# Performance work log

Hardware: AMD Instinct MI355X
Metric: run time of the kernel (lower is better)

The kernel has to match this reference:

```python
import jax, jax.numpy as jnp
import numpy as np

D_MODEL = 1024
NUM_HEADS = 16
HDIM = D_MODEL // NUM_HEADS
THETA = 10000.0


def setup_inputs() -> dict:
    key = jax.random.key(0)
    ks = jax.random.split(key, 5)
    bs, seq = 4, 2048
    std = np.sqrt(2.0 / (D_MODEL + D_MODEL))
    def w(k):
        # trunc_normal approximated by clipped normal (same distribution family)
        return jnp.clip(std * jax.random.normal(k, (D_MODEL, D_MODEL), jnp.float32), -3 * std, 3 * std)
    return {
        "x": jax.random.normal(ks[0], (bs, seq, D_MODEL), jnp.float32),
        "Wq": w(ks[1]), "Wk": w(ks[2]), "Wv": w(ks[3]), "Wo": w(ks[4]),
        "token_positions": jnp.arange(seq, dtype=jnp.int64),
    }


def _rope(x, token_positions):
    # x: (bs, H, S, hdim); rotate even/odd interleaved pairs
    inv_freq = THETA ** (-2.0 * jnp.arange(HDIM // 2, dtype=jnp.float32) / HDIM)
    freqs = token_positions.astype(jnp.float32)[:, None] * inv_freq[None, :]  # (S, hdim/2)
    cos, sin = jnp.cos(freqs), jnp.sin(freqs)
    x_even, x_odd = x[..., 0::2], x[..., 1::2]
    out_even = x_even * cos - x_odd * sin
    out_odd = x_odd * cos + x_even * sin
    # interleave back: stack on new last axis then reshape
    return jnp.stack([out_even, out_odd], axis=-1).reshape(x.shape)


def reference(x, Wq, Wk, Wv, Wo, token_positions):
    bs, seq, _ = x.shape
    q = (x @ Wq.T).reshape(bs, seq, NUM_HEADS, HDIM).transpose(0, 2, 1, 3)
    k = (x @ Wk.T).reshape(bs, seq, NUM_HEADS, HDIM).transpose(0, 2, 1, 3)
    v = (x @ Wv.T).reshape(bs, seq, NUM_HEADS, HDIM).transpose(0, 2, 1, 3)
    q = _rope(q, token_positions)
    k = _rope(k, token_positions)
    scores = jnp.einsum("bhsd,bhtd->bhst", q, k) / jnp.sqrt(jnp.float32(HDIM))
    mask = jnp.tril(jnp.ones((seq, seq), dtype=bool))
    scores = jnp.where(mask, scores, -jnp.inf)
    attn = jax.nn.softmax(scores, axis=-1)
    out = jnp.einsum("bhst,bhtd->bhsd", attn, v)
    out = out.transpose(0, 2, 1, 3).reshape(bs, seq, D_MODEL)
    return out @ Wo.T
```

## Files before the change

### kernel.cpp

```cpp
#include <hip/hip_runtime.h>
#include <hip/hip_fp16.h>

typedef _Float16 half8 __attribute__((ext_vector_type(8)));
typedef _Float16 half4 __attribute__((ext_vector_type(4)));
typedef _Float16 half2v __attribute__((ext_vector_type(2)));
typedef float f32x4 __attribute__((ext_vector_type(4)));
typedef float f32x8v __attribute__((ext_vector_type(8)));
typedef float f32x16 __attribute__((ext_vector_type(16)));

#define SEQ   2048
#define DM    1024
#define NH    16
#define HD    64
#define BSZ   4

#if __has_builtin(__builtin_amdgcn_exp2f)
#define EXP2(x) __builtin_amdgcn_exp2f(x)
#else
#define EXP2(x) exp2f(x)
#endif

#define QSCALE 0.1803368801f
#define ROPE_C 0.41524101186f

__device__ __forceinline__ void gload16(const void* g, void* l) {
  __builtin_amdgcn_global_load_lds((const __attribute__((address_space(1))) void*)g,
                                   (__attribute__((address_space(3))) void*)l,
                                   16, 0, 0);
}

__global__ void cvtAll(const float* __restrict__ x,
                       const float* __restrict__ s0, const float* __restrict__ s1,
                       const float* __restrict__ s2, const float* __restrict__ s3,
                       _Float16* __restrict__ xh, _Float16* __restrict__ dqkv,
                       _Float16* __restrict__ dO) {
  const int i = blockIdx.x * blockDim.x + threadIdx.x;
  const float* src;
  _Float16* dst;
  int idx;
  if (i < 2097152) {
    src = x; dst = xh; idx = i;
  } else {
    const int j = i - 2097152;
    const int which = j >> 18;
    idx = j & 262143;
    src = (which == 0) ? s0 : (which == 1) ? s1 : (which == 2) ? s2 : s3;
    dst = (which < 3) ? (dqkv + (long)which * (1u << 20)) : dO;
  }
  float4 v = ((const float4*)src)[idx];
  half4 o = { (_Float16)v.x, (_Float16)v.y, (_Float16)v.z, (_Float16)v.w };
  ((half4*)dst)[idx] = o;
}

template<int MODE>
__global__ __launch_bounds__(256)
void gemm_hk(const _Float16* __restrict__ A, const _Float16* __restrict__ B,
             _Float16* __restrict__ oQ, _Float16* __restrict__ oK,
             _Float16* __restrict__ oVt, float* __restrict__ oF,
             const int* __restrict__ tp) {
  __shared__ _Float16 As[2][128*32];
  __shared__ _Float16 Bs[2][128*32];
  const int tid  = threadIdx.x;
  const int wid  = tid >> 6, lane = tid & 63;
  const int wm   = wid >> 1, wn = wid & 1;
  const int fr   = lane & 15, fg = lane >> 4;
  const long m0  = (long)blockIdx.x * 128;
  const long n0  = (long)blockIdx.y * 128;
  const int sg    = (lane & 7) ^ ((lane >> 3) & 7);
  const int srowl = 2*(lane >> 3) + (sg >> 2);
  const int scol  = (sg & 3) * 8;
  const _Float16* ga0 = A + (m0 + wid*32 + srowl) * 1024 + scol;
  const _Float16* gb0 = B + (n0 + wid*32 + srowl) * 1024 + scol;
  const int lofs = wid*32*32;

  f32x4 acc[4][4] = {};

  auto ldfrag = [&](const char* base, int R) -> half8 {
    const int r = R & 31, r2 = r >> 1;
    return *(const half8*)(base + (R >> 5)*2048 + r2*128 +
                           (((((r & 1) << 2) | fg) ^ (r2 & 7)) << 4));
  };

  gload16(ga0,           &As[0][lofs]);
  gload16(ga0 + 16*1024, &As[0][lofs + 16*32]);
  gload16(gb0,           &Bs[0][lofs]);
  gload16(gb0 + 16*1024, &Bs[0][lofs + 16*32]);
  __syncthreads();

  int cur = 0;
  for (int k0 = 0; k0 < 1024; k0 += 32) {
    if (k0 + 32 < 1024) {
      gload16(ga0 + k0 + 32,           &As[cur^1][lofs]);
      gload16(ga0 + k0 + 32 + 16*1024, &As[cur^1][lofs + 16*32]);
      gload16(gb0 + k0 + 32,           &Bs[cur^1][lofs]);
      gload16(gb0 + k0 + 32 + 16*1024, &Bs[cur^1][lofs + 16*32]);
    }
    const char* Ab = (const char*)&As[cur][0];
    const char* Bb = (const char*)&Bs[cur][0];
    half8 af[4], bf[4];
#pragma unroll
    for (int i = 0; i < 4; ++i) {
      af[i] = ldfrag(Ab, wm*64 + i*16 + fr);
      bf[i] = ldfrag(Bb, wn*64 + i*16 + fr);
    }
    __builtin_amdgcn_s_setprio(1);
#pragma unroll
    for (int i = 0; i < 4; ++i)
#pragma unroll
      for (int j = 0; j < 4; ++j)
        acc[i][j] = __builtin_amdgcn_mfma_f32_16x16x32_f16(af[i], bf[j], acc[i][j], 0, 0, 0);
    __builtin_amdgcn_s_setprio(0);
    __syncthreads();
    cur ^= 1;
  }

  if (MODE == 0) {
    const int which = (int)(n0 >> 10);
    const int nloc0 = ((int)n0 & 1023) + wn*64;
    const bool odd = fr & 1;
#pragma unroll
    for (int i = 0; i < 4; ++i) {
      const long r0 = m0 + wm*64 + i*16 + fg*4;
      const int  bb = (int)(r0 >> 11);
      const int  s  = (int)(r0 & 2047);
#pragma unroll
      for (int j = 0; j < 4; ++j) {
        const int nl = nloc0 + j*16 + fr;
        const int h  = nl >> 6, d = nl & 63;
        const long bh = (long)(bb*NH + h);
        if (which == 2) {
          half4 pk = { (_Float16)acc[i][j][0], (_Float16)acc[i][j][1],
                       (_Float16)acc[i][j][2], (_Float16)acc[i][j][3] };
          *(half4*)&oVt[(bh*HD + d)*SEQ + s] = pk;
        } else {
          const float inv = exp2f(-ROPE_C * (float)(d >> 1));
#pragma unroll
          for (int r = 0; r < 4; ++r) {
            const float v = acc[i][j][r];
            const float p = __shfl_xor(v, 1);
            float sn, cs;
            __sincosf((float)tp[s + r] * inv, &sn, &cs);
            const float out = odd ? (v*cs + p*sn) : (v*cs - p*sn);
            if (which == 0)
              oQ[(bh*SEQ + s + r)*HD + d] = (_Float16)(out * QSCALE);
            else
              oK[(bh*SEQ + s + r)*HD + d] = (_Float16)out;
          }
        }
      }
    }
  } else {
#pragma unroll
    for (int i = 0; i < 4; ++i) {
      const long r0 = m0 + wm*64 + i*16 + fg*4;
#pragma unroll
      for (int j = 0; j < 4; ++j) {
        const long col = n0 + wn*64 + j*16 + fr;
#pragma unroll
        for (int r = 0; r < 4; ++r)
          oF[(r0 + r)*DM + col] = acc[i][j][r];
      }
    }
  }
}

__global__ __launch_bounds__(256, 2)
void fattn(const _Float16* __restrict__ Q, const _Float16* __restrict__ K,
           const _Float16* __restrict__ Vt, _Float16* __restrict__ O) {
  __shared__ _Float16 Ks[2][64*64];
  __shared__ _Float16 Vs[2][64*64];
  const int tid = threadIdx.x, wid = tid >> 6, lane = tid & 63;
  const int q31 = lane & 31, hi = lane >> 5;
  const int qp  = (q31 & 19) | ((q31 & 4) << 1) | ((q31 & 8) >> 1);
  const int bh = blockIdx.x, b = bh >> 4, h = bh & 15;
  const int y = blockIdx.y;
  const int qs_[2] = { (15 - y)*128 + wid*32, y*128 + wid*32 };
  const _Float16* Qb = Q + (long)bh * SEQ * HD;
  const _Float16* Kb = K + (long)bh * SEQ * HD;
  const _Float16* Vb = Vt + (long)bh * HD * SEQ;

  half8 qf[2][4];
#pragma unroll
  for (int s = 0; s < 2; ++s)
#pragma unroll
    for (int c = 0; c < 4; ++c)
      qf[s][c] = *(const half8*)&Qb[(qs_[s] + q31)*HD + c*16 + hi*8];

  f32x16 oacc[2][2] = {};
  float m_s[2] = { -1e30f, -1e30f }, l_s[2] = { 0.f, 0.f };

  const int srow = lane >> 3;
  const int sc16 = (lane & 7) ^ srow;
  const int r1 = wid*16 + srow, r2 = r1 + 8;

  const int nt = (15 - y)*2 + 2;

  gload16(Kb + (long)r1*HD + sc16*8, &Ks[0][(wid*16)*64]);
  gload16(Kb + (long)r2*HD + sc16*8, &Ks[0][(wid*16 + 8)*64]);
  gload16(Vb + (long)r1*SEQ + sc16*8, &Vs[0][(wid*16)*64]);
  gload16(Vb + (long)r2*SEQ + sc16*8, &Vs[0][(wid*16 + 8)*64]);
  __syncthreads();

  int cur = 0;
  for (int t = 0; t < nt; ++t) {
    const int kv0 = t * 64;

    if (t + 1 < nt) {
      const int nkv = kv0 + 64;
      gload16(Kb + (long)(nkv + r1)*HD + sc16*8, &Ks[cur^1][(wid*16)*64]);
      gload16(Kb + (long)(nkv + r2)*HD + sc16*8, &Ks[cur^1][(wid*16 + 8)*64]);
      gload16(Vb + (long)r1*SEQ + nkv + sc16*8,  &Vs[cur^1][(wid*16)*64]);
      gload16(Vb + (long)r2*SEQ + nkv + sc16*8,  &Vs[cur^1][(wid*16 + 8)*64]);
    }

    const char* Kc = (const char*)&Ks[cur][0];
    const char* Vc = (const char*)&Vs[cur][0];

#pragma unroll
    for (int hh = 0; hh < 2; ++hh) {
      const int kvb = kv0 + 32*hh;
#pragma unroll
      for (int s = 0; s < 2; ++s) {
        const int qs0 = qs_[s];
        if (kvb > qs0 + 31) continue;

        f32x16 sa = {};
        __builtin_amdgcn_s_setprio(1);
#pragma unroll
        for (int c = 0; c < 4; ++c) {
          const int row = 32*hh + qp;
          const half8 kf = *(const half8*)(Kc + row*128 + ((c*32 + hi*16) ^ ((row & 7) << 4)));
          sa = __builtin_amdgcn_mfma_f32_32x32x16_f16(kf, qf[s][c], sa, 0, 0, 0);
        }
        __builtin_amdgcn_s_setprio(0);

        if (kvb + 31 > qs0) {
          const int thr = qs0 + q31 - kvb - 8*hi;
#pragma unroll
          for (int r = 0; r < 16; ++r) {
            const int cr = (r & 3) + 4*((r >> 2) & 1) + 16*(r >> 3);
            if (cr > thr) sa[r] = -1e30f;
          }
        }

        f32x8v mx8;
#pragma unroll
        for (int i = 0; i < 8; ++i) mx8[i] = fmaxf(sa[i], sa[i+8]);
        f32x4 mx4;
#pragma unroll
        for (int i = 0; i < 4; ++i) mx4[i] = fmaxf(mx8[i], mx8[i+4]);
        float pm = fmaxf(fmaxf(mx4[0], mx4[1]), fmaxf(mx4[2], mx4[3]));
        pm = fmaxf(pm, __shfl_xor(pm, 32));

        if (!__all(pm <= m_s[s] + 8.0f)) {
          const float mn = fmaxf(m_s[s], pm);
          const float fac = EXP2(m_s[s] - mn);
          m_s[s] = mn;
          l_s[s] *= fac;
          oacc[s][0] *= fac;
          oacc[s][1] *= fac;
        }
        const float mrow = m_s[s];

#pragma unroll
        for (int r = 0; r < 16; ++r) sa[r] = EXP2(sa[r] - mrow);

        f32x8v s8;
#pragma unroll
        for (int i = 0; i < 8; ++i) s8[i] = sa[i] + sa[i+8];
        f32x4 s4v;
#pragma unroll
        for (int i = 0; i < 4; ++i) s4v[i] = s8[i] + s8[i+4];
        float ps = (s4v[0] + s4v[1]) + (s4v[2] + s4v[3]);
        ps += __shfl_xor(ps, 32);
        l_s[s] += ps;

        half8 pf0, pf1;
#pragma unroll
        for (int g = 0; g < 4; ++g) {
          half2v t0 = (half2v)__builtin_amdgcn_cvt_pkrtz(sa[2*g],   sa[2*g+1]);
          half2v t1 = (half2v)__builtin_amdgcn_cvt_pkrtz(sa[8+2*g], sa[8+2*g+1]);
          pf0[2*g]   = t0[0];  pf0[2*g+1] = t0[1];
          pf1[2*g]   = t1[0];  pf1[2*g+1] = t1[1];
        }

        __builtin_amdgcn_s_setprio(1);
#pragma unroll
        for (int ks = 0; ks < 2; ++ks) {
          const half8 pf = ks ? pf1 : pf0;
#pragma unroll
          for (int nd = 0; nd < 2; ++nd) {
            const int row = nd*32 + q31;
            const half8 vf = *(const half8*)(Vc + row*128 +
                              ((hh*64 + ks*32 + hi*16) ^ ((row & 7) << 4)));
            oacc[s][nd] = __builtin_amdgcn_mfma_f32_32x32x16_f16(vf, pf, oacc[s][nd], 0, 0, 0);
          }
        }
        __builtin_amdgcn_s_setprio(0);
      }
    }

    __syncthreads();
    cur ^= 1;
  }

#pragma unroll
  for (int s = 0; s < 2; ++s) {
    const float rl = __builtin_amdgcn_rcpf(l_s[s]);
    _Float16* orow = O + ((long)b*SEQ + (qs_[s] + q31))*DM + h*64;
#pragma unroll
    for (int nd = 0; nd < 2; ++nd)
#pragma unroll
      for (int g = 0; g < 4; ++g) {
        half2v lo  = (half2v)__builtin_amdgcn_cvt_pkrtz(oacc[s][nd][4*g+0]*rl, oacc[s][nd][4*g+1]*rl);
        half2v hi2 = (half2v)__builtin_amdgcn_cvt_pkrtz(oacc[s][nd][4*g+2]*rl, oacc[s][nd][4*g+3]*rl);
        half4 o4 = __builtin_shufflevector(lo, hi2, 0, 1, 2, 3);
        *(half4*)&orow[nd*32 + g*8 + 4*hi] = o4;
      }
  }
}

extern "C" void kernel_launch(void* const* d_in, const int* in_sizes, int n_in,
                              void* d_out, int out_size, void* d_ws, size_t ws_size,
                              hipStream_t stream) {
  const float* x  = (const float*)d_in[0];
  const float* Wq = (const float*)d_in[1];
  const float* Wk = (const float*)d_in[2];
  const float* Wv = (const float*)d_in[3];
  const float* Wo = (const float*)d_in[4];
  const int*   tp = (const int*)d_in[5];
  float* out = (float*)d_out;

  char* ws = (char*)d_ws;
  _Float16* xh   = (_Float16*)(ws);
  _Float16* Wqkv = (_Float16*)(ws + (16u << 20));
  _Float16* Woh  = (_Float16*)(ws + (22u << 20));
  _Float16* Qb   = (_Float16*)(ws + (24u << 20));
  _Float16* Kb   = (_Float16*)(ws + (40u << 20));
  _Float16* Vtb  = (_Float16*)(ws + (56u << 20));
  _Float16* attn = (_Float16*)(ws + (72u << 20));

  cvtAll<<<12288, 256, 0, stream>>>(x, Wq, Wk, Wv, Wo, xh, Wqkv, Woh);

  gemm_hk<0><<<dim3(64, 24), 256, 0, stream>>>(xh, Wqkv, Qb, Kb, Vtb, nullptr, tp);
  fattn<<<dim3(64, 8), 256, 0, stream>>>(Qb, Kb, Vtb, attn);
  gemm_hk<1><<<dim3(64, 8), 256, 0, stream>>>(attn, Woh, nullptr, nullptr, nullptr, out, nullptr);
}
```

Baseline: 167.5 us.

## Replace QKV projection GEMM with 256x256-tile, 8-wave ping-pong pipelined kernel

The fused QKV projection (with RoPE epilogue) now runs in a new kernel that uses 256x256 output tiles, 512 threads and 128KB of dynamic LDS. Loads are double-buffered with 64-wide K steps, split into halves, interleaved with MFMA phases and gated by explicit barriers and vmcnt waits. The aim is to raise arithmetic intensity per tile and hide global-load latency behind MFMA work. The cost is more register and LDS pressure, fewer blocks (384), and brittle hand-tuned wait counts. The output projection is split into its own non-templated kernel.

```diff
diff --git a/kernel.cpp b/kernel.cpp
--- a/kernel.cpp
+++ b/kernel.cpp
@@ -52,12 +52,139 @@
   ((half4*)dst)[idx] = o;
 }
 
-template<int MODE>
+__global__ __launch_bounds__(512, 2)
+void gemm8p(const _Float16* __restrict__ A, const _Float16* __restrict__ B,
+            _Float16* __restrict__ oQ, _Float16* __restrict__ oK,
+            _Float16* __restrict__ oVt, const int* __restrict__ tp) {
+  extern __shared__ char lds[];
+  const int tid = threadIdx.x;
+  const int w = tid >> 6, lane = tid & 63;
+  const int wm = w >> 2, wnn = w & 3;
+  const int fr = lane & 15, fg = lane >> 4;
+  const long m0 = (long)blockIdx.x * 256;
+  const long n0 = (long)blockIdx.y * 256;
+  const int sg = (lane & 7) ^ ((lane >> 3) & 7);
+  const int srowl = 2*(lane >> 3) + (sg >> 2);
+  const int scol = (sg & 3) * 8;
+
+  f32x4 acc[8][4] = {};
+
+  auto stA = [&](int b, int kh, int b2, int kt) {
+    const int c = b2*8 + w;
+    gload16(A + (m0 + 32*(c>>1) + 16*(c&1) + srowl)*1024 + kt*64 + kh*32 + scol,
+            lds + b*65536 + kh*16384 + c*1024);
+  };
+  auto stB = [&](int b, int kh, int b2, int kt) {
+    const int c = b2*8 + w;
+    gload16(B + (n0 + 32*(c>>1) + 16*(c&1) + srowl)*1024 + kt*64 + kh*32 + scol,
+            lds + b*65536 + 32768 + kh*16384 + c*1024);
+  };
+  auto ldfrag = [&](const char* base, int R) -> half8 {
+    const int r = R & 31, r2 = r >> 1;
+    return *(const half8*)(base + (R >> 5)*2048 + r2*128 +
+                           (((((r & 1) << 2) | fg) ^ (r2 & 7)) << 4));
+  };
+
+  half8 af[4], bf[4];
+
+#define READ_AF(b, mq, kh) _Pragma("unroll") for (int mi = 0; mi < 4; ++mi) \
+    af[mi] = ldfrag(lds + (b)*65536 + (kh)*16384, wm*128 + (mq)*64 + mi*16 + fr);
+#define READ_BF(b, kh) _Pragma("unroll") for (int ni = 0; ni < 4; ++ni) \
+    bf[ni] = ldfrag(lds + (b)*65536 + 32768 + (kh)*16384, wnn*64 + ni*16 + fr);
+#define MFMA16(mq) __builtin_amdgcn_s_setprio(1); \
+    _Pragma("unroll") for (int mi = 0; mi < 4; ++mi) \
+    _Pragma("unroll") for (int ni = 0; ni < 4; ++ni) \
+      acc[(mq)*4+mi][ni] = __builtin_amdgcn_mfma_f32_16x16x32_f16(af[mi], bf[ni], \
+                             acc[(mq)*4+mi][ni], 0, 0, 0); \
+    __builtin_amdgcn_s_setprio(0);
+#define BAR() __builtin_amdgcn_s_barrier()
+
+  stA(0,0,0,0); stA(0,0,1,0); stA(0,1,0,0); stA(0,1,1,0);
+  stB(0,0,0,0); stB(0,0,1,0); stB(0,1,0,0); stB(0,1,1,0);
+  stB(1,0,0,1); stB(1,0,1,1);
+  stA(1,0,0,1); stA(1,0,1,1);
+  stB(1,1,0,1); stB(1,1,1,1);
+  asm volatile("s_waitcnt vmcnt(6)" ::: "memory");
+  BAR();
+
+  for (int i = 0; i < 8; ++i) {
+    const int t2 = 2*i + 2, t3 = 2*i + 3;
+    const bool st = (i < 7);
+    READ_AF(0,0,0) READ_BF(0,0)
+    stA(1,1,0,2*i+1); stA(1,1,1,2*i+1);
+    BAR(); MFMA16(0) BAR();
+    READ_AF(0,1,0)
+    if (st) { stB(0,0,0,t2); stB(0,0,1,t2); }
+    BAR(); MFMA16(1) BAR();
+    READ_AF(0,0,1) READ_BF(0,1)
+    if (st) { stA(0,0,0,t2); stA(0,0,1,t2); }
+    BAR(); MFMA16(0) BAR();
+    READ_AF(0,1,1)
+    if (st) { stB(0,1,0,t2); stB(0,1,1,t2); }
+    BAR(); MFMA16(1)
+    if (st) { asm volatile("s_waitcnt vmcnt(6)" ::: "memory"); }
+    else    { asm volatile("s_waitcnt vmcnt(0)" ::: "memory"); }
+    BAR();
+    READ_AF(1,0,0) READ_BF(1,0)
+    if (st) { stA(0,1,0,t2); stA(0,1,1,t2); }
+    BAR(); MFMA16(0) BAR();
+    READ_AF(1,1,0)
+    if (st) { stB(1,0,0,t3); stB(1,0,1,t3); }
+    BAR(); MFMA16(1) BAR();
+    READ_AF(1,0,1) READ_BF(1,1)
+    if (st) { stA(1,0,0,t3); stA(1,0,1,t3); }
+    BAR(); MFMA16(0) BAR();
+    READ_AF(1,1,1)
+    if (st) { stB(1,1,0,t3); stB(1,1,1,t3); }
+    BAR(); MFMA16(1)
+    if (st) { asm volatile("s_waitcnt vmcnt(6)" ::: "memory"); }
+    else    { asm volatile("s_waitcnt vmcnt(0)" ::: "memory"); }
+    BAR();
+  }
+#undef READ_AF
+#undef READ_BF
+#undef MFMA16
+#undef BAR
+
+  const int which = (int)(n0 >> 10);
+  const int nloc0 = ((int)n0 & 1023) + wnn*64;
+  const bool odd = fr & 1;
+#pragma unroll
+  for (int mi = 0; mi < 8; ++mi) {
+    const long r0 = m0 + wm*128 + mi*16 + fg*4;
+    const int  bb = (int)(r0 >> 11);
+    const int  s  = (int)(r0 & 2047);
+#pragma unroll
+    for (int ni = 0; ni < 4; ++ni) {
+      const int nl = nloc0 + ni*16 + fr;
+      const int h  = nl >> 6, d = nl & 63;
+      const long bh = (long)(bb*NH + h);
+      if (which == 2) {
+        half4 pk = { (_Float16)acc[mi][ni][0], (_Float16)acc[mi][ni][1],
+                     (_Float16)acc[mi][ni][2], (_Float16)acc[mi][ni][3] };
+        *(half4*)&oVt[(bh*HD + d)*SEQ + s] = pk;
+      } else {
+        const float inv = exp2f(-ROPE_C * (float)(d >> 1));
+#pragma unroll
+        for (int r = 0; r < 4; ++r) {
+          const float v = acc[mi][ni][r];
+          const float p = __shfl_xor(v, 1);
+          float sn, cs;
+          __sincosf((float)tp[s + r] * inv, &sn, &cs);
+          const float out = odd ? (v*cs + p*sn) : (v*cs - p*sn);
+          if (which == 0)
+            oQ[(bh*SEQ + s + r)*HD + d] = (_Float16)(out * QSCALE);
+          else
+            oK[(bh*SEQ + s + r)*HD + d] = (_Float16)out;
+        }
+      }
+    }
+  }
+}
+
 __global__ __launch_bounds__(256)
-void gemm_hk(const _Float16* __restrict__ A, const _Float16* __restrict__ B,
-             _Float16* __restrict__ oQ, _Float16* __restrict__ oK,
-             _Float16* __restrict__ oVt, float* __restrict__ oF,
-             const int* __restrict__ tp) {
+void gemm_out(const _Float16* __restrict__ A, const _Float16* __restrict__ B,
+              float* __restrict__ oF) {
   __shared__ _Float16 As[2][128*32];
   __shared__ _Float16 Bs[2][128*32];
   const int tid  = threadIdx.x;
@@ -114,52 +241,15 @@
     cur ^= 1;
   }
 
-  if (MODE == 0) {
-    const int which = (int)(n0 >> 10);
-    const int nloc0 = ((int)n0 & 1023) + wn*64;
-    const bool odd = fr & 1;
-#pragma unroll
-    for (int i = 0; i < 4; ++i) {
-      const long r0 = m0 + wm*64 + i*16 + fg*4;
-      const int  bb = (int)(r0 >> 11);
-      const int  s  = (int)(r0 & 2047);
-#pragma unroll
-      for (int j = 0; j < 4; ++j) {
-        const int nl = nloc0 + j*16 + fr;
-        const int h  = nl >> 6, d = nl & 63;
-        const long bh = (long)(bb*NH + h);
-        if (which == 2) {
-          half4 pk = { (_Float16)acc[i][j][0], (_Float16)acc[i][j][1],
-                       (_Float16)acc[i][j][2], (_Float16)acc[i][j][3] };
-          *(half4*)&oVt[(bh*HD + d)*SEQ + s] = pk;
-        } else {
-          const float inv = exp2f(-ROPE_C * (float)(d >> 1));
-#pragma unroll
-          for (int r = 0; r < 4; ++r) {
-            const float v = acc[i][j][r];
-            const float p = __shfl_xor(v, 1);
-            float sn, cs;
-            __sincosf((float)tp[s + r] * inv, &sn, &cs);
-            const float out = odd ? (v*cs + p*sn) : (v*cs - p*sn);
-            if (which == 0)
-              oQ[(bh*SEQ + s + r)*HD + d] = (_Float16)(out * QSCALE);
-            else
-              oK[(bh*SEQ + s + r)*HD + d] = (_Float16)out;
-          }
-        }
-      }
-    }
-  } else {
-#pragma unroll
-    for (int i = 0; i < 4; ++i) {
-      const long r0 = m0 + wm*64 + i*16 + fg*4;
-#pragma unroll
-      for (int j = 0; j < 4; ++j) {
-        const long col = n0 + wn*64 + j*16 + fr;
-#pragma unroll
-        for (int r = 0; r < 4; ++r)
-          oF[(r0 + r)*DM + col] = acc[i][j][r];
-      }
+#pragma unroll
+  for (int i = 0; i < 4; ++i) {
+    const long r0 = m0 + wm*64 + i*16 + fg*4;
+#pragma unroll
+    for (int j = 0; j < 4; ++j) {
+      const long col = n0 + wn*64 + j*16 + fr;
+#pragma unroll
+      for (int r = 0; r < 4; ++r)
+        oF[(r0 + r)*DM + col] = acc[i][j][r];
     }
   }
 }
@@ -342,7 +432,7 @@
 
   cvtAll<<<12288, 256, 0, stream>>>(x, Wq, Wk, Wv, Wo, xh, Wqkv, Woh);
 
-  gemm_hk<0><<<dim3(64, 24), 256, 0, stream>>>(xh, Wqkv, Qb, Kb, Vtb, nullptr, tp);
+  gemm8p<<<dim3(32, 12), 512, 131072, stream>>>(xh, Wqkv, Qb, Kb, Vtb, tp);
   fattn<<<dim3(64, 8), 256, 0, stream>>>(Qb, Kb, Vtb, attn);
-  gemm_hk<1><<<dim3(64, 8), 256, 0, stream>>>(attn, Woh, nullptr, nullptr, nullptr, out, nullptr);
-}
+  gemm_out<<<dim3(64, 8), 256, 0, stream>>>(attn, Woh, out);
+}
```

Result: no change. 170.7 us (+1.9%).
